# Kernel tuning notes

Measured on AMD Instinct MI355X. Metric: run time of the kernel, lower is better.

## Reference

```python
import jax, jax.numpy as jnp
import numpy as np

N = 50000      # nodes
E = 1600000    # edges (avg degree 32)
DIN, DH, DOUT = 256, 128, 64


def gcn_conv(x, W, b, row, col, w, n):
    """One GCNConv layer (self-loops already appended to row/col/w).
    row = source nodes, col = target nodes; aggregate at targets."""
    xw = x @ W                                        # [n, d_out]
    deg = jax.ops.segment_sum(w, col, num_segments=n)  # in-degree weighted
    dinv = jnp.where(deg > 0, jax.lax.rsqrt(deg), 0.0)
    norm = dinv[row] * w * dinv[col]                  # [E+n]
    msg = norm[:, None] * xw[row]                     # [E+n, d_out] gather
    out = jax.ops.segment_sum(msg, col, num_segments=n)
    return out + b


def setup_inputs() -> dict:
    key = jax.random.key(0)
    k = jax.random.split(key, 6)
    x = jax.random.normal(k[0], (N, DIN), dtype=jnp.float32)
    edge_index = jax.random.randint(k[1], (2, E), 0, N)
    edge_weight = jax.random.uniform(k[2], (E,), dtype=jnp.float32)
    W1 = jax.random.normal(k[3], (DIN, DH), dtype=jnp.float32) * (1.0 / np.sqrt(DIN))
    b1 = jnp.zeros((DH,), dtype=jnp.float32)
    W2 = jax.random.normal(k[4], (DH, DOUT), dtype=jnp.float32) * (1.0 / np.sqrt(DH))
    b2 = jnp.zeros((DOUT,), dtype=jnp.float32)
    return {"x": x, "edge_index": edge_index, "edge_weight": edge_weight,
            "W1": W1, "b1": b1, "W2": W2, "b2": b2}


def reference(x, edge_index, edge_weight, W1, b1, W2, b2):
    n = x.shape[0]
    loops = jnp.arange(n, dtype=edge_index.dtype)
    row = jnp.concatenate([edge_index[0], loops])
    col = jnp.concatenate([edge_index[1], loops])
    w = jnp.concatenate([edge_weight, jnp.ones((n,), dtype=edge_weight.dtype)])
    h = gcn_conv(x, W1, b1, row, col, w, n)
    h = jax.nn.relu(h)
    # dropout(p=0.2) is identity in eval mode
    h = gcn_conv(h, W2, b2, row, col, w, n)
    return jax.nn.log_softmax(h, axis=-1)
```

## Files before the change

kernel.cpp:

```cpp
#include <hip/hip_runtime.h>
#include <hip/hip_bf16.h>
#include <hip/hip_fp16.h>
#include <cstddef>


#define DIN 256
#define DH  128
#define DOUT 64
#define NPB 100
#define NBMAX 512

typedef __bf16 bf16x8 __attribute__((ext_vector_type(8)));
typedef float f32x4 __attribute__((ext_vector_type(4)));

__device__ __forceinline__ float bflo(unsigned u) { return __uint_as_float(u << 16); }
__device__ __forceinline__ float bfhi(unsigned u) { return __uint_as_float(u & 0xffff0000u); }
__device__ __forceinline__ unsigned short f2bf(float f) {
    unsigned u = __float_as_uint(f);
    unsigned r = (u + 0x7fffu + ((u >> 16) & 1u)) >> 16;
    return (unsigned short)r;
}
__device__ __forceinline__ float wdec(unsigned rec) {
    return __half2float(__ushort_as_half((unsigned short)(rec >> 16)));
}

__global__ void prep_w_kernel(const float* __restrict__ W1, const float* __restrict__ W2,
                              unsigned short* __restrict__ wt1, unsigned short* __restrict__ wt2) {
    int i = blockIdx.x * 256 + threadIdx.x;
    if (i < DH * DIN) {
        int nn = i >> 8, k = i & 255;
        wt1[i] = f2bf(W1[k * DH + nn]);
    } else {
        int j = i - DH * DIN;
        if (j < DOUT * DH) {
            int nn = j >> 7, k = j & 127;
            wt2[j] = f2bf(W2[k * DOUT + nn]);
        }
    }
}

__launch_bounds__(256)
__global__ void hist_kernel(const int* __restrict__ col, int* __restrict__ bh,
                            int E, int Ec, int NB) {
    __shared__ int hist[NBMAX];
    int p = blockIdx.x, t = threadIdx.x;
    for (int b = t; b < NB; b += 256) hist[b] = 0;
    __syncthreads();
    int s = p * Ec, e = min(s + Ec, E);
    for (int i = s + t; i < e; i += 256) atomicAdd(&hist[col[i] / NPB], 1);
    __syncthreads();
    for (int b = t; b < NB; b += 256) bh[p * NB + b] = hist[b];
}

__launch_bounds__(512)
__global__ void colscan_kernel(int* __restrict__ bh, int* __restrict__ btotal,
                               int P, int NB) {
    __shared__ int arr[512];
    int b = blockIdx.x, t = threadIdx.x;
    arr[t] = (t < P) ? bh[t * NB + b] : 0;
    __syncthreads();
    for (int off = 1; off < 512; off <<= 1) {
        int v = (t >= off) ? arr[t - off] : 0;
        __syncthreads();
        arr[t] += v;
        __syncthreads();
    }
    int excl = (t == 0) ? 0 : arr[t - 1];
    if (t < P) bh[t * NB + b] = excl;
    if (t == P - 1) btotal[b] = arr[t];
}

__launch_bounds__(512)
__global__ void basescan_kernel(const int* __restrict__ btotal, int* __restrict__ bbase,
                                int* __restrict__ rowptr, int NB, int n, int E) {
    __shared__ int arr[512];
    int t = threadIdx.x;
    arr[t] = (t < NB) ? btotal[t] : 0;
    __syncthreads();
    for (int off = 1; off < 512; off <<= 1) {
        int v = (t >= off) ? arr[t - off] : 0;
        __syncthreads();
        arr[t] += v;
        __syncthreads();
    }
    int excl = (t == 0) ? 0 : arr[t - 1];
    if (t <= NB) bbase[t] = excl;
    if (t == 511) rowptr[n] = E;
}

__launch_bounds__(256)
__global__ void scatter_kernel(const int* __restrict__ row, const int* __restrict__ col,
                               const float* __restrict__ w, const int* __restrict__ bh,
                               const int* __restrict__ bbase, int2* __restrict__ part,
                               int E, int Ec, int NB) {
    __shared__ int cur[NBMAX];
    int p = blockIdx.x, t = threadIdx.x;
    for (int b = t; b < NB; b += 256) cur[b] = bbase[b] + bh[p * NB + b];
    __syncthreads();
    int s = p * Ec, e = min(s + Ec, E);
    for (int i = s + t; i < e; i += 256) {
        int c = col[i];
        int r = row[i];
        int b = c / NPB;
        int pos = atomicAdd(&cur[b], 1);
        part[pos] = make_int2(r | ((c - b * NPB) << 16), __float_as_int(w[i]));
    }
}

__launch_bounds__(256)
__global__ void bucket_csr_kernel(const int2* __restrict__ part, const int* __restrict__ bbase,
                                  float* __restrict__ dinv, int* __restrict__ rowptr,
                                  unsigned* __restrict__ final_e, int n) {
    __shared__ int   hist[NPB];
    __shared__ float wsum[NPB];
    __shared__ int   nbase[NPB];
    __shared__ int   cur[NPB];
    int b = blockIdx.x, t = threadIdx.x;
    if (t < NPB) { hist[t] = 0; wsum[t] = 0.0f; }
    __syncthreads();
    int s = bbase[b], e = bbase[b + 1];
    for (int i = s + t; i < e; i += 256) {
        int2 rec = part[i];
        int cl = rec.x >> 16;
        atomicAdd(&hist[cl], 1);
        atomicAdd(&wsum[cl], __int_as_float(rec.y));
    }
    __syncthreads();
    if (t == 0) {
        int run = 0;
        for (int k = 0; k < NPB; ++k) { nbase[k] = run; run += hist[k]; }
    }
    __syncthreads();
    if (t < NPB) {
        int node = b * NPB + t;
        if (node < n) {
            dinv[node] = rsqrtf(1.0f + wsum[t]);
            rowptr[node] = s + nbase[t];
        }
        cur[t] = nbase[t];
    }
    __syncthreads();
    for (int i = s + t; i < e; i += 256) {
        int2 rec = part[i];
        int cl = rec.x >> 16;
        int q = s + atomicAdd(&cur[cl], 1);
        unsigned short ws = __half_as_ushort(__float2half_rn(__int_as_float(rec.y)));
        final_e[q] = ((unsigned)rec.x & 0xffffu) | ((unsigned)ws << 16);
    }
}

template <int K, int M>
__launch_bounds__(256)
__global__ void gemm_mfma_kernel(const float* __restrict__ A,
                                 const unsigned short* __restrict__ Wt,
                                 const float* __restrict__ scale,
                                 unsigned short* __restrict__ C, int N) {
    constexpr int BK = 64, LD = BK + 8;
    constexpr int WN = M / 4;
    constexpr int NT = WN / 16;
    constexpr int CLD = M + 8;
    constexpr int SM = (64 * LD + M * LD) > (64 * CLD) ? (64 * LD + M * LD) : (64 * CLD);
    __shared__ unsigned short smem[SM];
    __shared__ float sdv[64];
    unsigned short* As = smem;
    unsigned short* Bs = smem + 64 * LD;

    const int tid = threadIdx.x;
    const int row0 = blockIdx.x * 64;
    const int lane = tid & 63;
    const int quad = lane >> 4, r16 = lane & 15;
    const int n0 = (tid >> 6) * WN;

    if (tid < 64) {
        int r = row0 + tid;
        sdv[tid] = (r < N) ? scale[r] : 0.0f;
    }

    f32x4 acc[4][NT];
#pragma unroll
    for (int mt = 0; mt < 4; ++mt)
#pragma unroll
        for (int nt = 0; nt < NT; ++nt)
            acc[mt][nt] = (f32x4){0.f, 0.f, 0.f, 0.f};

    for (int k0 = 0; k0 < K; k0 += BK) {
#pragma unroll
        for (int j = 0; j < 4; ++j) {
            int idx = tid + j * 256;
            int m = idx >> 4;
            int q = idx & 15;
            int gr = row0 + m;
            float4 v = make_float4(0.f, 0.f, 0.f, 0.f);
            if (gr < N) v = *(const float4*)&A[(size_t)gr * K + k0 + q * 4];
            ushort4 s4;
            s4.x = f2bf(v.x); s4.y = f2bf(v.y); s4.z = f2bf(v.z); s4.w = f2bf(v.w);
            *(ushort4*)&As[m * LD + q * 4] = s4;
        }
#pragma unroll
        for (int j = 0; j < M * 8 / 256; ++j) {
            int idx = tid + j * 256;
            int nn = idx >> 3;
            int q = idx & 7;
            uint4 v = *(const uint4*)&Wt[(size_t)nn * K + k0 + q * 8];
            *(uint4*)&Bs[nn * LD + q * 8] = v;
        }
        __syncthreads();
#pragma unroll
        for (int ks = 0; ks < BK / 32; ++ks) {
            bf16x8 af[4], bfr[NT];
#pragma unroll
            for (int nt = 0; nt < NT; ++nt)
                bfr[nt] = *(const bf16x8*)&Bs[(n0 + nt * 16 + r16) * LD + ks * 32 + quad * 8];
#pragma unroll
            for (int mt = 0; mt < 4; ++mt)
                af[mt] = *(const bf16x8*)&As[(mt * 16 + r16) * LD + ks * 32 + quad * 8];
#pragma unroll
            for (int mt = 0; mt < 4; ++mt)
#pragma unroll
                for (int nt = 0; nt < NT; ++nt)
                    acc[mt][nt] = __builtin_amdgcn_mfma_f32_16x16x32_bf16(
                        af[mt], bfr[nt], acc[mt][nt], 0, 0, 0);
        }
        __syncthreads();
    }
    unsigned short* Cs = smem;
#pragma unroll
    for (int mt = 0; mt < 4; ++mt) {
#pragma unroll
        for (int i = 0; i < 4; ++i) {
            int r = mt * 16 + quad * 4 + i;
            float sc = sdv[r];
#pragma unroll
            for (int nt = 0; nt < NT; ++nt)
                Cs[r * CLD + n0 + nt * 16 + r16] = f2bf(acc[mt][nt][i] * sc);
        }
    }
    __syncthreads();
#pragma unroll
    for (int j = 0; j < 64 * M / 8 / 256; ++j) {
        int idx = tid + j * 256;
        int r = idx / (M / 8);
        int q = idx % (M / 8);
        int gr = row0 + r;
        if (gr < N) {
            uint4 v = *(const uint4*)&Cs[r * CLD + q * 8];
            *(uint4*)&C[(size_t)gr * M + q * 8] = v;
        }
    }
}

#define ACC8(v, wgt)                                            \
    a0 += (wgt) * bflo((v).x); a1 += (wgt) * bfhi((v).x);       \
    a2 += (wgt) * bflo((v).y); a3 += (wgt) * bfhi((v).y);       \
    a4 += (wgt) * bflo((v).z); a5 += (wgt) * bfhi((v).z);       \
    a6 += (wgt) * bflo((v).w); a7 += (wgt) * bfhi((v).w);

__launch_bounds__(256, 6)
__global__ void agg1_kernel(const unsigned short* __restrict__ xw,
                            const int* __restrict__ rowptr,
                            const unsigned* __restrict__ edge,
                            const float* __restrict__ dinv,
                            const float* __restrict__ bias,
                            float* __restrict__ out, int n) {
    int node = blockIdx.x * 4 + (threadIdx.x >> 6);
    if (node >= n) return;
    int lane = threadIdx.x & 63;
    int qw = lane >> 4, sub = lane & 15;
    const char* xb = (const char*)xw;
    const unsigned ssub = (unsigned)sub << 4;
    float di = dinv[node];

    float a0 = 0.f, a1 = 0.f, a2 = 0.f, a3 = 0.f;
    float a4 = 0.f, a5 = 0.f, a6 = 0.f, a7 = 0.f;
    if (qw == 0) {
        uint4 u = *(const uint4*)(xb + (((unsigned)node) << 8) + ssub);
        a0 = bflo(u.x); a1 = bfhi(u.x); a2 = bflo(u.y); a3 = bfhi(u.y);
        a4 = bflo(u.z); a5 = bfhi(u.z); a6 = bflo(u.w); a7 = bfhi(u.w);
    }

    int p = rowptr[node], p1 = rowptr[node + 1];
    int sb = 4 * qw;
    unsigned r0, r1, r2, r3;
    uint4 v0, v1, v2, v3;
    bool have = (p + 16 <= p1);
    if (have) {
        const unsigned* rp = edge + p + sb;
        r0 = __builtin_nontemporal_load(rp);
        r1 = __builtin_nontemporal_load(rp + 1);
        r2 = __builtin_nontemporal_load(rp + 2);
        r3 = __builtin_nontemporal_load(rp + 3);
        v0 = *(const uint4*)(xb + ((r0 & 0xffffu) << 8) + ssub);
        v1 = *(const uint4*)(xb + ((r1 & 0xffffu) << 8) + ssub);
        v2 = *(const uint4*)(xb + ((r2 & 0xffffu) << 8) + ssub);
        v3 = *(const uint4*)(xb + ((r3 & 0xffffu) << 8) + ssub);
    }
#pragma unroll 1
    while (have) {
        p += 16;
        bool havn = (p + 16 <= p1);
        unsigned m0 = 0, m1 = 0, m2 = 0, m3 = 0;
        uint4 u0 = {0,0,0,0}, u1 = {0,0,0,0}, u2 = {0,0,0,0}, u3 = {0,0,0,0};
        if (havn) {
            const unsigned* rp = edge + p + sb;
            m0 = __builtin_nontemporal_load(rp);
            m1 = __builtin_nontemporal_load(rp + 1);
            m2 = __builtin_nontemporal_load(rp + 2);
            m3 = __builtin_nontemporal_load(rp + 3);
            u0 = *(const uint4*)(xb + ((m0 & 0xffffu) << 8) + ssub);
            u1 = *(const uint4*)(xb + ((m1 & 0xffffu) << 8) + ssub);
            u2 = *(const uint4*)(xb + ((m2 & 0xffffu) << 8) + ssub);
            u3 = *(const uint4*)(xb + ((m3 & 0xffffu) << 8) + ssub);
        }
        float w0 = wdec(r0), w1 = wdec(r1), w2 = wdec(r2), w3 = wdec(r3);
        ACC8(v0, w0); ACC8(v1, w1); ACC8(v2, w2); ACC8(v3, w3);
        r0 = m0; r1 = m1; r2 = m2; r3 = m3;
        v0 = u0; v1 = u1; v2 = u2; v3 = u3;
        have = havn;
    }
    int rem = p1 - p;
    if (rem > 0) {
        int last = p1 - 1, b = p + sb;
        unsigned e0 = edge[min(b, last)],     e1 = edge[min(b + 1, last)];
        unsigned e2 = edge[min(b + 2, last)], e3 = edge[min(b + 3, last)];
        float w0 = (b     <= last) ? wdec(e0) : 0.f;
        float w1 = (b + 1 <= last) ? wdec(e1) : 0.f;
        float w2 = (b + 2 <= last) ? wdec(e2) : 0.f;
        float w3 = (b + 3 <= last) ? wdec(e3) : 0.f;
        uint4 t0 = *(const uint4*)(xb + ((e0 & 0xffffu) << 8) + ssub);
        uint4 t1 = *(const uint4*)(xb + ((e1 & 0xffffu) << 8) + ssub);
        uint4 t2 = *(const uint4*)(xb + ((e2 & 0xffffu) << 8) + ssub);
        uint4 t3 = *(const uint4*)(xb + ((e3 & 0xffffu) << 8) + ssub);
        ACC8(t0, w0); ACC8(t1, w1); ACC8(t2, w2); ACC8(t3, w3);
    }
    a0 += __shfl_xor(a0, 16); a0 += __shfl_xor(a0, 32);
    a1 += __shfl_xor(a1, 16); a1 += __shfl_xor(a1, 32);
    a2 += __shfl_xor(a2, 16); a2 += __shfl_xor(a2, 32);
    a3 += __shfl_xor(a3, 16); a3 += __shfl_xor(a3, 32);
    a4 += __shfl_xor(a4, 16); a4 += __shfl_xor(a4, 32);
    a5 += __shfl_xor(a5, 16); a5 += __shfl_xor(a5, 32);
    a6 += __shfl_xor(a6, 16); a6 += __shfl_xor(a6, 32);
    a7 += __shfl_xor(a7, 16); a7 += __shfl_xor(a7, 32);
    if (qw < 2) {
        float4 b = ((const float4*)bias)[2 * sub + qw];
        f32x4 o;
        if (qw == 0) { o.x = a0; o.y = a1; o.z = a2; o.w = a3; }
        else         { o.x = a4; o.y = a5; o.z = a6; o.w = a7; }
        o.x = fmaxf(di * o.x + b.x, 0.f);
        o.y = fmaxf(di * o.y + b.y, 0.f);
        o.z = fmaxf(di * o.z + b.z, 0.f);
        o.w = fmaxf(di * o.w + b.w, 0.f);
        __builtin_nontemporal_store(o, (f32x4*)out + (size_t)node * 32 + 2 * sub + qw);
    }
}

__launch_bounds__(256, 6)
__global__ void agg2_kernel(const unsigned short* __restrict__ xw,
                            const int* __restrict__ rowptr,
                            const unsigned* __restrict__ edge,
                            const float* __restrict__ dinv,
                            const float* __restrict__ bias,
                            float* __restrict__ out, int n) {
    int node = blockIdx.x * 4 + (threadIdx.x >> 6);
    if (node >= n) return;
    int lane = threadIdx.x & 63;
    int oct = lane >> 3, sub = lane & 7;
    const char* xb = (const char*)xw;
    const unsigned ssub = (unsigned)sub << 4;
    float di = dinv[node];

    float a0 = 0.f, a1 = 0.f, a2 = 0.f, a3 = 0.f;
    float a4 = 0.f, a5 = 0.f, a6 = 0.f, a7 = 0.f;
    if (oct == 0) {
        uint4 u = *(const uint4*)(xb + (((unsigned)node) << 7) + ssub);
        a0 = bflo(u.x); a1 = bfhi(u.x); a2 = bflo(u.y); a3 = bfhi(u.y);
        a4 = bflo(u.z); a5 = bfhi(u.z); a6 = bflo(u.w); a7 = bfhi(u.w);
    }

    int p = rowptr[node], p1 = rowptr[node + 1];
    int sb = 4 * oct;
    unsigned r0, r1, r2, r3;
    uint4 v0, v1, v2, v3;
    bool have = (p + 32 <= p1);
    if (have) {
        const unsigned* rp = edge + p + sb;
        r0 = __builtin_nontemporal_load(rp);
        r1 = __builtin_nontemporal_load(rp + 1);
        r2 = __builtin_nontemporal_load(rp + 2);
        r3 = __builtin_nontemporal_load(rp + 3);
        v0 = *(const uint4*)(xb + ((r0 & 0xffffu) << 7) + ssub);
        v1 = *(const uint4*)(xb + ((r1 & 0xffffu) << 7) + ssub);
        v2 = *(const uint4*)(xb + ((r2 & 0xffffu) << 7) + ssub);
        v3 = *(const uint4*)(xb + ((r3 & 0xffffu) << 7) + ssub);
    }
#pragma unroll 1
    while (have) {
        p += 32;
        bool havn = (p + 32 <= p1);
        unsigned m0 = 0, m1 = 0, m2 = 0, m3 = 0;
        uint4 u0 = {0,0,0,0}, u1 = {0,0,0,0}, u2 = {0,0,0,0}, u3 = {0,0,0,0};
        if (havn) {
            const unsigned* rp = edge + p + sb;
            m0 = __builtin_nontemporal_load(rp);
            m1 = __builtin_nontemporal_load(rp + 1);
            m2 = __builtin_nontemporal_load(rp + 2);
            m3 = __builtin_nontemporal_load(rp + 3);
            u0 = *(const uint4*)(xb + ((m0 & 0xffffu) << 7) + ssub);
            u1 = *(const uint4*)(xb + ((m1 & 0xffffu) << 7) + ssub);
            u2 = *(const uint4*)(xb + ((m2 & 0xffffu) << 7) + ssub);
            u3 = *(const uint4*)(xb + ((m3 & 0xffffu) << 7) + ssub);
        }
        float w0 = wdec(r0), w1 = wdec(r1), w2 = wdec(r2), w3 = wdec(r3);
        ACC8(v0, w0); ACC8(v1, w1); ACC8(v2, w2); ACC8(v3, w3);
        r0 = m0; r1 = m1; r2 = m2; r3 = m3;
        v0 = u0; v1 = u1; v2 = u2; v3 = u3;
        have = havn;
    }
    int rem = p1 - p;
    if (rem > 0) {
        int last = p1 - 1, b = p + sb;
        unsigned e0 = edge[min(b, last)],     e1 = edge[min(b + 1, last)];
        unsigned e2 = edge[min(b + 2, last)], e3 = edge[min(b + 3, last)];
        float w0 = (b     <= last) ? wdec(e0) : 0.f;
        float w1 = (b + 1 <= last) ? wdec(e1) : 0.f;
        float w2 = (b + 2 <= last) ? wdec(e2) : 0.f;
        float w3 = (b + 3 <= last) ? wdec(e3) : 0.f;
        uint4 t0 = *(const uint4*)(xb + ((e0 & 0xffffu) << 7) + ssub);
        uint4 t1 = *(const uint4*)(xb + ((e1 & 0xffffu) << 7) + ssub);
        uint4 t2 = *(const uint4*)(xb + ((e2 & 0xffffu) << 7) + ssub);
        uint4 t3 = *(const uint4*)(xb + ((e3 & 0xffffu) << 7) + ssub);
        ACC8(t0, w0); ACC8(t1, w1); ACC8(t2, w2); ACC8(t3, w3);
    }
    a0 += __shfl_xor(a0, 8); a0 += __shfl_xor(a0, 16); a0 += __shfl_xor(a0, 32);
    a1 += __shfl_xor(a1, 8); a1 += __shfl_xor(a1, 16); a1 += __shfl_xor(a1, 32);
    a2 += __shfl_xor(a2, 8); a2 += __shfl_xor(a2, 16); a2 += __shfl_xor(a2, 32);
    a3 += __shfl_xor(a3, 8); a3 += __shfl_xor(a3, 16); a3 += __shfl_xor(a3, 32);
    a4 += __shfl_xor(a4, 8); a4 += __shfl_xor(a4, 16); a4 += __shfl_xor(a4, 32);
    a5 += __shfl_xor(a5, 8); a5 += __shfl_xor(a5, 16); a5 += __shfl_xor(a5, 32);
    a6 += __shfl_xor(a6, 8); a6 += __shfl_xor(a6, 16); a6 += __shfl_xor(a6, 32);
    a7 += __shfl_xor(a7, 8); a7 += __shfl_xor(a7, 16); a7 += __shfl_xor(a7, 32);
    const float4* bp = (const float4*)bias;
    float4 bl = bp[2 * sub], bh = bp[2 * sub + 1];
    a0 = di * a0 + bl.x; a1 = di * a1 + bl.y; a2 = di * a2 + bl.z; a3 = di * a3 + bl.w;
    a4 = di * a4 + bh.x; a5 = di * a5 + bh.y; a6 = di * a6 + bh.z; a7 = di * a7 + bh.w;
    float m = fmaxf(fmaxf(fmaxf(a0, a1), fmaxf(a2, a3)),
                    fmaxf(fmaxf(a4, a5), fmaxf(a6, a7)));
    m = fmaxf(m, __shfl_xor(m, 4));
    m = fmaxf(m, __shfl_xor(m, 2));
    m = fmaxf(m, __shfl_xor(m, 1));
    float s = __expf(a0 - m) + __expf(a1 - m) + __expf(a2 - m) + __expf(a3 - m)
            + __expf(a4 - m) + __expf(a5 - m) + __expf(a6 - m) + __expf(a7 - m);
    s += __shfl_xor(s, 4);
    s += __shfl_xor(s, 2);
    s += __shfl_xor(s, 1);
    float lse = m + __logf(s);
    if (oct < 2) {
        f32x4 o;
        if (oct == 0) { o.x = a0 - lse; o.y = a1 - lse; o.z = a2 - lse; o.w = a3 - lse; }
        else          { o.x = a4 - lse; o.y = a5 - lse; o.z = a6 - lse; o.w = a7 - lse; }
        __builtin_nontemporal_store(o, (f32x4*)out + (size_t)node * 16 + 2 * sub + oct);
    }
}

extern "C" void kernel_launch(void* const* d_in, const int* in_sizes, int n_in,
                              void* d_out, int out_size, void* d_ws, size_t ws_size,
                              hipStream_t stream) {
    const float* x  = (const float*)d_in[0];
    const int*   ei = (const int*)d_in[1];
    const float* ew = (const float*)d_in[2];
    const float* W1 = (const float*)d_in[3];
    const float* b1 = (const float*)d_in[4];
    const float* W2 = (const float*)d_in[5];
    const float* b2 = (const float*)d_in[6];
    float* out = (float*)d_out;

    const int n = in_sizes[0] / DIN;
    const int E = in_sizes[2];
    const int* row = ei;
    const int* col = ei + E;

    const int NB = (n + NPB - 1) / NPB;
    const int P  = NB;
    const int Ec = (E + P - 1) / P;

    char* ptr = (char*)d_ws;
    auto alloc = [&](size_t bytes) -> void* {
        void* r = (void*)ptr;
        ptr += (bytes + 255) & ~(size_t)255;
        return r;
    };
    int*   bh     = (int*)  alloc((size_t)P * NB * 4);
    int*   btotal = (int*)  alloc((size_t)NB * 4);
    int*   bbase  = (int*)  alloc((size_t)(NB + 1) * 4);
    int*   rowptr = (int*)  alloc((size_t)(n + 1) * 4);
    float* dinv   = (float*)alloc((size_t)n * 4);
    unsigned* edge = (unsigned*)alloc((size_t)E * 4);
    unsigned short* xw1 = (unsigned short*)alloc((size_t)n * DH * 2);
    unsigned short* wt1 = (unsigned short*)alloc((size_t)DH * DIN * 2);
    unsigned short* wt2 = (unsigned short*)alloc((size_t)DOUT * DH * 2);
    char* tail = (char*)alloc((size_t)n * DH * 4);
    int2*  part = (int2*)tail;
    float* h1   = (float*)tail;
    unsigned short* xw2 = xw1;

    const int nb_g = (n + 63) / 64;
    const int nb_a = (n + 3) / 4;

    prep_w_kernel<<<(DH * DIN + DOUT * DH + 255) / 256, 256, 0, stream>>>(W1, W2, wt1, wt2);
    hist_kernel<<<P, 256, 0, stream>>>(col, bh, E, Ec, NB);
    colscan_kernel<<<NB, 512, 0, stream>>>(bh, btotal, P, NB);
    basescan_kernel<<<1, 512, 0, stream>>>(btotal, bbase, rowptr, NB, n, E);
    scatter_kernel<<<P, 256, 0, stream>>>(row, col, ew, bh, bbase, part, E, Ec, NB);
    bucket_csr_kernel<<<NB, 256, 0, stream>>>(part, bbase, dinv, rowptr, edge, n);

    gemm_mfma_kernel<DIN, DH><<<nb_g, 256, 0, stream>>>(x, wt1, dinv, xw1, n);
    agg1_kernel<<<nb_a, 256, 0, stream>>>(xw1, rowptr, edge, dinv, b1, h1, n);
    gemm_mfma_kernel<DH, DOUT><<<nb_g, 256, 0, stream>>>(h1, wt2, dinv, xw2, n);
    agg2_kernel<<<nb_a, 256, 0, stream>>>(xw2, rowptr, edge, dinv, b2, out, n);
}
```

Measured before the change: 276.1 us.

## Merge CSR-build stages with first GEMM and fold source dinv into edge weights

Several small preprocessing kernels are folded into two multi-role launches. Weight transposition runs alongside the histogram, and the first GEMM shares a launch with the per-bucket scan and the dinv computation. Weighted degree now comes from global float atomics in the histogram pass, and the base scan moves into each scatter block. The source-side dinv scaling moves from the GEMM epilogue into the fp16 edge weight, with the self-loop term scaled in the aggregation kernels. The aim is fewer launches and serialization gaps and letting the GEMM overlap the CSR build, at the cost of global atomic contention on wsum and a redundant scan in every scatter block.

```diff
diff --git a/kernel.cpp b/kernel.cpp
--- a/kernel.cpp
+++ b/kernel.cpp
@@ -24,157 +24,57 @@
     return __half2float(__ushort_as_half((unsigned short)(rec >> 16)));
 }
 
-__global__ void prep_w_kernel(const float* __restrict__ W1, const float* __restrict__ W2,
-                              unsigned short* __restrict__ wt1, unsigned short* __restrict__ wt2) {
-    int i = blockIdx.x * 256 + threadIdx.x;
-    if (i < DH * DIN) {
-        int nn = i >> 8, k = i & 255;
-        wt1[i] = f2bf(W1[k * DH + nn]);
+__launch_bounds__(256)
+__global__ void kernelA(const int* __restrict__ col, const float* __restrict__ ew,
+                        int* __restrict__ bh, float* __restrict__ wsum,
+                        int E, int Ec, int NB, int P,
+                        const float* __restrict__ W1, const float* __restrict__ W2,
+                        unsigned short* __restrict__ wt1, unsigned short* __restrict__ wt2) {
+    int blk = blockIdx.x, t = threadIdx.x;
+    if (blk < P) {
+        __shared__ int hist[NBMAX];
+        for (int b = t; b < NB; b += 256) hist[b] = 0;
+        __syncthreads();
+        int s = blk * Ec, e = min(s + Ec, E);
+        for (int i = s + t; i < e; i += 256) {
+            int c = col[i];
+            atomicAdd(&hist[c / NPB], 1);
+            atomicAdd(&wsum[c], ew[i]);
+        }
+        __syncthreads();
+        for (int b = t; b < NB; b += 256) bh[blk * NB + b] = hist[b];
     } else {
-        int j = i - DH * DIN;
-        if (j < DOUT * DH) {
-            int nn = j >> 7, k = j & 127;
-            wt2[j] = f2bf(W2[k * DOUT + nn]);
-        }
-    }
-}
-
-__launch_bounds__(256)
-__global__ void hist_kernel(const int* __restrict__ col, int* __restrict__ bh,
-                            int E, int Ec, int NB) {
-    __shared__ int hist[NBMAX];
-    int p = blockIdx.x, t = threadIdx.x;
-    for (int b = t; b < NB; b += 256) hist[b] = 0;
-    __syncthreads();
-    int s = p * Ec, e = min(s + Ec, E);
-    for (int i = s + t; i < e; i += 256) atomicAdd(&hist[col[i] / NPB], 1);
-    __syncthreads();
-    for (int b = t; b < NB; b += 256) bh[p * NB + b] = hist[b];
-}
-
-__launch_bounds__(512)
-__global__ void colscan_kernel(int* __restrict__ bh, int* __restrict__ btotal,
-                               int P, int NB) {
-    __shared__ int arr[512];
-    int b = blockIdx.x, t = threadIdx.x;
-    arr[t] = (t < P) ? bh[t * NB + b] : 0;
-    __syncthreads();
-    for (int off = 1; off < 512; off <<= 1) {
-        int v = (t >= off) ? arr[t - off] : 0;
-        __syncthreads();
-        arr[t] += v;
-        __syncthreads();
-    }
-    int excl = (t == 0) ? 0 : arr[t - 1];
-    if (t < P) bh[t * NB + b] = excl;
-    if (t == P - 1) btotal[b] = arr[t];
-}
-
-__launch_bounds__(512)
-__global__ void basescan_kernel(const int* __restrict__ btotal, int* __restrict__ bbase,
-                                int* __restrict__ rowptr, int NB, int n, int E) {
-    __shared__ int arr[512];
-    int t = threadIdx.x;
-    arr[t] = (t < NB) ? btotal[t] : 0;
-    __syncthreads();
-    for (int off = 1; off < 512; off <<= 1) {
-        int v = (t >= off) ? arr[t - off] : 0;
-        __syncthreads();
-        arr[t] += v;
-        __syncthreads();
-    }
-    int excl = (t == 0) ? 0 : arr[t - 1];
-    if (t <= NB) bbase[t] = excl;
-    if (t == 511) rowptr[n] = E;
-}
-
-__launch_bounds__(256)
-__global__ void scatter_kernel(const int* __restrict__ row, const int* __restrict__ col,
-                               const float* __restrict__ w, const int* __restrict__ bh,
-                               const int* __restrict__ bbase, int2* __restrict__ part,
-                               int E, int Ec, int NB) {
-    __shared__ int cur[NBMAX];
-    int p = blockIdx.x, t = threadIdx.x;
-    for (int b = t; b < NB; b += 256) cur[b] = bbase[b] + bh[p * NB + b];
-    __syncthreads();
-    int s = p * Ec, e = min(s + Ec, E);
-    for (int i = s + t; i < e; i += 256) {
-        int c = col[i];
-        int r = row[i];
-        int b = c / NPB;
-        int pos = atomicAdd(&cur[b], 1);
-        part[pos] = make_int2(r | ((c - b * NPB) << 16), __float_as_int(w[i]));
-    }
-}
-
-__launch_bounds__(256)
-__global__ void bucket_csr_kernel(const int2* __restrict__ part, const int* __restrict__ bbase,
-                                  float* __restrict__ dinv, int* __restrict__ rowptr,
-                                  unsigned* __restrict__ final_e, int n) {
-    __shared__ int   hist[NPB];
-    __shared__ float wsum[NPB];
-    __shared__ int   nbase[NPB];
-    __shared__ int   cur[NPB];
-    int b = blockIdx.x, t = threadIdx.x;
-    if (t < NPB) { hist[t] = 0; wsum[t] = 0.0f; }
-    __syncthreads();
-    int s = bbase[b], e = bbase[b + 1];
-    for (int i = s + t; i < e; i += 256) {
-        int2 rec = part[i];
-        int cl = rec.x >> 16;
-        atomicAdd(&hist[cl], 1);
-        atomicAdd(&wsum[cl], __int_as_float(rec.y));
-    }
-    __syncthreads();
-    if (t == 0) {
-        int run = 0;
-        for (int k = 0; k < NPB; ++k) { nbase[k] = run; run += hist[k]; }
-    }
-    __syncthreads();
-    if (t < NPB) {
-        int node = b * NPB + t;
-        if (node < n) {
-            dinv[node] = rsqrtf(1.0f + wsum[t]);
-            rowptr[node] = s + nbase[t];
-        }
-        cur[t] = nbase[t];
-    }
-    __syncthreads();
-    for (int i = s + t; i < e; i += 256) {
-        int2 rec = part[i];
-        int cl = rec.x >> 16;
-        int q = s + atomicAdd(&cur[cl], 1);
-        unsigned short ws = __half_as_ushort(__float2half_rn(__int_as_float(rec.y)));
-        final_e[q] = ((unsigned)rec.x & 0xffffu) | ((unsigned)ws << 16);
+        int i = (blk - P) * 256 + t;
+        if (i < DH * DIN) {
+            int nn = i >> 8, k = i & 255;
+            wt1[i] = f2bf(W1[k * DH + nn]);
+        } else {
+            int j = i - DH * DIN;
+            if (j < DOUT * DH) {
+                int nn = j >> 7, k = j & 127;
+                wt2[j] = f2bf(W2[k * DOUT + nn]);
+            }
+        }
     }
 }
 
 template <int K, int M>
-__launch_bounds__(256)
-__global__ void gemm_mfma_kernel(const float* __restrict__ A,
-                                 const unsigned short* __restrict__ Wt,
-                                 const float* __restrict__ scale,
-                                 unsigned short* __restrict__ C, int N) {
+__device__ __forceinline__ void gemm_body(const float* __restrict__ A,
+                                          const unsigned short* __restrict__ Wt,
+                                          unsigned short* __restrict__ C,
+                                          int N, int blk, int tid, char* smemRaw) {
     constexpr int BK = 64, LD = BK + 8;
     constexpr int WN = M / 4;
     constexpr int NT = WN / 16;
     constexpr int CLD = M + 8;
-    constexpr int SM = (64 * LD + M * LD) > (64 * CLD) ? (64 * LD + M * LD) : (64 * CLD);
-    __shared__ unsigned short smem[SM];
-    __shared__ float sdv[64];
+    unsigned short* smem = (unsigned short*)smemRaw;
     unsigned short* As = smem;
     unsigned short* Bs = smem + 64 * LD;
 
-    const int tid = threadIdx.x;
-    const int row0 = blockIdx.x * 64;
+    const int row0 = blk * 64;
     const int lane = tid & 63;
     const int quad = lane >> 4, r16 = lane & 15;
     const int n0 = (tid >> 6) * WN;
-
-    if (tid < 64) {
-        int r = row0 + tid;
-        sdv[tid] = (r < N) ? scale[r] : 0.0f;
-    }
 
     f32x4 acc[4][NT];
 #pragma unroll
@@ -229,10 +129,9 @@
 #pragma unroll
         for (int i = 0; i < 4; ++i) {
             int r = mt * 16 + quad * 4 + i;
-            float sc = sdv[r];
 #pragma unroll
             for (int nt = 0; nt < NT; ++nt)
-                Cs[r * CLD + n0 + nt * 16 + r16] = f2bf(acc[mt][nt][i] * sc);
+                Cs[r * CLD + n0 + nt * 16 + r16] = f2bf(acc[mt][nt][i]);
         }
     }
     __syncthreads();
@@ -247,6 +146,129 @@
             *(uint4*)&C[(size_t)gr * M + q * 8] = v;
         }
     }
+}
+
+__launch_bounds__(256)
+__global__ void kernelB(const float* __restrict__ x, const unsigned short* __restrict__ wt1,
+                        unsigned short* __restrict__ xw1, int n,
+                        int* __restrict__ bh, int* __restrict__ btotal, int P, int NB,
+                        int nbg1, const float* __restrict__ wsum, float* __restrict__ dinv) {
+    __shared__ char smemRaw[(64 * 72 + DH * 72) * 2];
+    int blk = blockIdx.x, t = threadIdx.x;
+    if (blk < nbg1) {
+        gemm_body<DIN, DH>(x, wt1, xw1, n, blk, t, smemRaw);
+    } else if (blk < nbg1 + NB) {
+        int b = blk - nbg1;
+        int* ps = (int*)smemRaw;
+        int i0 = 2 * t, i1 = 2 * t + 1;
+        int x0 = (i0 < P) ? bh[i0 * NB + b] : 0;
+        int x1 = (i1 < P) ? bh[i1 * NB + b] : 0;
+        int s = x0 + x1;
+        ps[t] = s;
+        __syncthreads();
+        for (int off = 1; off < 256; off <<= 1) {
+            int v = (t >= off) ? ps[t - off] : 0;
+            __syncthreads();
+            ps[t] += v;
+            __syncthreads();
+        }
+        int excl = ps[t] - s;
+        if (i0 < P) bh[i0 * NB + b] = excl;
+        if (i1 < P) bh[i1 * NB + b] = excl + x0;
+        if (t == 255) btotal[b] = ps[255];
+    } else {
+        int i = (blk - nbg1 - NB) * 256 + t;
+        if (i < n) dinv[i] = rsqrtf(1.0f + wsum[i]);
+    }
+}
+
+__launch_bounds__(256)
+__global__ void scatter_kernel(const int* __restrict__ row, const int* __restrict__ col,
+                               const float* __restrict__ w, const int* __restrict__ bh,
+                               const int* __restrict__ btotal, int* __restrict__ bbase,
+                               int* __restrict__ rowptr, int2* __restrict__ part,
+                               int E, int Ec, int NB, int n) {
+    __shared__ int ps[256];
+    __shared__ int bb[NBMAX];
+    __shared__ int cur[NBMAX];
+    int p = blockIdx.x, t = threadIdx.x;
+    int i0 = 2 * t, i1 = 2 * t + 1;
+    int x0 = (i0 < NB) ? btotal[i0] : 0;
+    int x1 = (i1 < NB) ? btotal[i1] : 0;
+    int s = x0 + x1;
+    ps[t] = s;
+    __syncthreads();
+    for (int off = 1; off < 256; off <<= 1) {
+        int v = (t >= off) ? ps[t - off] : 0;
+        __syncthreads();
+        ps[t] += v;
+        __syncthreads();
+    }
+    int excl = ps[t] - s;
+    if (i0 < NB) bb[i0] = excl;
+    if (i1 < NB) bb[i1] = excl + x0;
+    __syncthreads();
+    for (int b = t; b < NB; b += 256) cur[b] = bb[b] + bh[p * NB + b];
+    if (p == 0) {
+        if (i0 < NB) bbase[i0] = bb[i0];
+        if (i1 < NB) bbase[i1] = bb[i1];
+        if (t == 255) { bbase[NB] = ps[255]; rowptr[n] = E; }
+    }
+    __syncthreads();
+    int s0 = p * Ec, e = min(s0 + Ec, E);
+    for (int i = s0 + t; i < e; i += 256) {
+        int c = col[i];
+        int r = row[i];
+        int b = c / NPB;
+        int pos = atomicAdd(&cur[b], 1);
+        part[pos] = make_int2(r | ((c - b * NPB) << 16), __float_as_int(w[i]));
+    }
+}
+
+__launch_bounds__(256)
+__global__ void bucket_csr_kernel(const int2* __restrict__ part, const int* __restrict__ bbase,
+                                  const float* __restrict__ dinv, int* __restrict__ rowptr,
+                                  unsigned* __restrict__ final_e, int n) {
+    __shared__ int   hist[NPB];
+    __shared__ int   nbase[NPB];
+    __shared__ int   cur[NPB];
+    int b = blockIdx.x, t = threadIdx.x;
+    if (t < NPB) hist[t] = 0;
+    __syncthreads();
+    int s = bbase[b], e = bbase[b + 1];
+    for (int i = s + t; i < e; i += 256) {
+        int2 rec = part[i];
+        atomicAdd(&hist[rec.x >> 16], 1);
+    }
+    __syncthreads();
+    if (t == 0) {
+        int run = 0;
+        for (int k = 0; k < NPB; ++k) { nbase[k] = run; run += hist[k]; }
+    }
+    __syncthreads();
+    if (t < NPB) {
+        int node = b * NPB + t;
+        if (node < n) rowptr[node] = s + nbase[t];
+        cur[t] = nbase[t];
+    }
+    __syncthreads();
+    for (int i = s + t; i < e; i += 256) {
+        int2 rec = part[i];
+        int cl = rec.x >> 16;
+        int q = s + atomicAdd(&cur[cl], 1);
+        int src = rec.x & 0xffff;
+        float wp = __int_as_float(rec.y) * dinv[src];
+        unsigned short ws = __half_as_ushort(__float2half_rn(wp));
+        final_e[q] = (unsigned)src | ((unsigned)ws << 16);
+    }
+}
+
+template <int K, int M>
+__launch_bounds__(256)
+__global__ void gemm_kernel(const float* __restrict__ A, const unsigned short* __restrict__ Wt,
+                            unsigned short* __restrict__ C, int N) {
+    __shared__ char smemRaw[(64 * 72 + M * 72) * 2];
+    gemm_body<K, M>(A, Wt, C, N, blockIdx.x, threadIdx.x, smemRaw);
 }
 
 #define ACC8(v, wgt)                                            \
@@ -274,8 +296,8 @@
     float a4 = 0.f, a5 = 0.f, a6 = 0.f, a7 = 0.f;
     if (qw == 0) {
         uint4 u = *(const uint4*)(xb + (((unsigned)node) << 8) + ssub);
-        a0 = bflo(u.x); a1 = bfhi(u.x); a2 = bflo(u.y); a3 = bfhi(u.y);
-        a4 = bflo(u.z); a5 = bfhi(u.z); a6 = bflo(u.w); a7 = bfhi(u.w);
+        a0 = di * bflo(u.x); a1 = di * bfhi(u.x); a2 = di * bflo(u.y); a3 = di * bfhi(u.y);
+        a4 = di * bflo(u.z); a5 = di * bfhi(u.z); a6 = di * bflo(u.w); a7 = di * bfhi(u.w);
     }
 
     int p = rowptr[node], p1 = rowptr[node + 1];
@@ -372,8 +394,8 @@
     float a4 = 0.f, a5 = 0.f, a6 = 0.f, a7 = 0.f;
     if (oct == 0) {
         uint4 u = *(const uint4*)(xb + (((unsigned)node) << 7) + ssub);
-        a0 = bflo(u.x); a1 = bfhi(u.x); a2 = bflo(u.y); a3 = bfhi(u.y);
-        a4 = bflo(u.z); a5 = bfhi(u.z); a6 = bflo(u.w); a7 = bfhi(u.w);
+        a0 = di * bflo(u.x); a1 = di * bfhi(u.x); a2 = di * bflo(u.y); a3 = di * bfhi(u.y);
+        a4 = di * bflo(u.z); a5 = di * bfhi(u.z); a6 = di * bflo(u.w); a7 = di * bfhi(u.w);
     }
 
     int p = rowptr[node], p1 = rowptr[node + 1];
@@ -493,6 +515,7 @@
     int*   bbase  = (int*)  alloc((size_t)(NB + 1) * 4);
     int*   rowptr = (int*)  alloc((size_t)(n + 1) * 4);
     float* dinv   = (float*)alloc((size_t)n * 4);
+    float* wsum   = (float*)alloc((size_t)n * 4);
     unsigned* edge = (unsigned*)alloc((size_t)E * 4);
     unsigned short* xw1 = (unsigned short*)alloc((size_t)n * DH * 2);
     unsigned short* wt1 = (unsigned short*)alloc((size_t)DH * DIN * 2);
@@ -502,18 +525,17 @@
     float* h1   = (float*)tail;
     unsigned short* xw2 = xw1;
 
-    const int nb_g = (n + 63) / 64;
+    const int nbg1 = (n + 63) / 64;
+    const int ndiv = (n + 255) / 256;
     const int nb_a = (n + 3) / 4;
-
-    prep_w_kernel<<<(DH * DIN + DOUT * DH + 255) / 256, 256, 0, stream>>>(W1, W2, wt1, wt2);
-    hist_kernel<<<P, 256, 0, stream>>>(col, bh, E, Ec, NB);
-    colscan_kernel<<<NB, 512, 0, stream>>>(bh, btotal, P, NB);
-    basescan_kernel<<<1, 512, 0, stream>>>(btotal, bbase, rowptr, NB, n, E);
-    scatter_kernel<<<P, 256, 0, stream>>>(row, col, ew, bh, bbase, part, E, Ec, NB);
+    const int prepb = (DH * DIN + DOUT * DH + 255) / 256;
+
+    hipMemsetAsync(wsum, 0, (size_t)n * 4, stream);
+    kernelA<<<P + prepb, 256, 0, stream>>>(col, ew, bh, wsum, E, Ec, NB, P, W1, W2, wt1, wt2);
+    kernelB<<<nbg1 + NB + ndiv, 256, 0, stream>>>(x, wt1, xw1, n, bh, btotal, P, NB, nbg1, wsum, dinv);
+    scatter_kernel<<<P, 256, 0, stream>>>(row, col, ew, bh, btotal, bbase, rowptr, part, E, Ec, NB, n);
     bucket_csr_kernel<<<NB, 256, 0, stream>>>(part, bbase, dinv, rowptr, edge, n);
-
-    gemm_mfma_kernel<DIN, DH><<<nb_g, 256, 0, stream>>>(x, wt1, dinv, xw1, n);
     agg1_kernel<<<nb_a, 256, 0, stream>>>(xw1, rowptr, edge, dinv, b1, h1, n);
-    gemm_mfma_kernel<DH, DOUT><<<nb_g, 256, 0, stream>>>(h1, wt2, dinv, xw2, n);
+    gemm_kernel<DH, DOUT><<<nbg1, 256, 0, stream>>>(h1, wt2, xw2, n);
     agg2_kernel<<<nb_a, 256, 0, stream>>>(xw2, rowptr, edge, dinv, b2, out, n);
 }
```

Result: slower. 354.0 us (+28.2%).
